# Kernel tuning notes

Measured on AMD Instinct MI355X. Metric: run time of the kernel, lower is better.

## Reference

```python
import jax, jax.numpy as jnp
import numpy as np

N, E, D, C, H1 = 50000, 800000, 128, 8, 2


def setup_inputs() -> dict:
    key = jax.random.key(0)
    ks = jax.random.split(key, 14)
    s = lambda k, sh: (jax.random.normal(k, sh, jnp.float32) * 0.05)
    return {
        "x": jax.random.normal(ks[0], (N, D), jnp.float32),
        "edge_index": jax.random.randint(ks[1], (2, E), 0, N, dtype=jnp.int32),
        # conv1: GATConv(D, D, heads=2, concat=True)
        "W1": s(ks[2], (D, H1 * D)),
        "att1_src": s(ks[3], (H1, D)),
        "att1_dst": s(ks[4], (H1, D)),
        "b1": s(ks[5], (H1 * D,)),
        # conv2: GATConv(2D, D, heads=1, concat=False)
        "W2": s(ks[6], (H1 * D, D)),
        "att2_src": s(ks[7], (1, D)),
        "att2_dst": s(ks[8], (1, D)),
        "b2": s(ks[9], (D,)),
        # MLP head
        "Wm1": s(ks[10], (D, D)),
        "bm1": s(ks[11], (D,)),
        "Wm2": s(ks[12], (D, C)),
        "bm2": s(ks[13], (C,)),
    }


def gat_conv(x, src, dst, W, a_src, a_dst, b, heads, out_ch, concat):
    """PyG GATConv (eval mode): self-loops added by caller, softmax over
    edges grouped by destination node, negative_slope=0.2."""
    n = x.shape[0]
    h = (x @ W).reshape(n, heads, out_ch)              # [N,H,F]
    alpha_src = jnp.einsum('nhf,hf->nh', h, a_src)     # [N,H]
    alpha_dst = jnp.einsum('nhf,hf->nh', h, a_dst)     # [N,H]
    e = jax.nn.leaky_relu(alpha_src[src] + alpha_dst[dst], 0.2)  # [E,H]
    e_max = jax.ops.segment_max(e, dst, num_segments=n)
    ex = jnp.exp(e - e_max[dst])
    denom = jax.ops.segment_sum(ex, dst, num_segments=n)
    alpha = ex / jnp.maximum(denom[dst], 1e-16)        # [E,H]
    out = jax.ops.segment_sum(h[src] * alpha[:, :, None], dst, num_segments=n)
    out = out.reshape(n, heads * out_ch) if concat else out.mean(axis=1)
    return out + b


def reference(x, edge_index, W1, att1_src, att1_dst, b1,
              W2, att2_src, att2_dst, b2, Wm1, bm1, Wm2, bm2):
    n = x.shape[0]
    loop = jnp.arange(n, dtype=edge_index.dtype)
    src = jnp.concatenate([edge_index[0], loop])  # add_self_loops=True
    dst = jnp.concatenate([edge_index[1], loop])
    h = jax.nn.elu(gat_conv(x, src, dst, W1, att1_src, att1_dst, b1, H1, D, True))
    h = jax.nn.elu(gat_conv(h, src, dst, W2, att2_src, att2_dst, b2, 1, D, False))
    h = jax.nn.relu(h @ Wm1 + bm1)
    return jax.nn.relu(h @ Wm2 + bm2)
```

## Files before the change

kernel.cpp:

```cpp
#include <hip/hip_runtime.h>
#include <hip/hip_bf16.h>


__device__ __forceinline__ float lrelu(float x){ return x > 0.f ? x : 0.2f*x; }
__device__ __forceinline__ float elu_f(float x){ return x > 0.f ? x : __expf(x) - 1.f; }
__device__ __forceinline__ unsigned short f2bf(float f){
  __hip_bfloat16 h = __float2bfloat16(f);
  return *reinterpret_cast<unsigned short*>(&h);
}
__device__ __forceinline__ float bflo(unsigned int u){ return __uint_as_float(u << 16); }
__device__ __forceinline__ float bfhi(unsigned int u){ return __uint_as_float(u & 0xffff0000u); }
__device__ __forceinline__ unsigned int packbf(float a, float b){
  return (unsigned int)f2bf(a) | ((unsigned int)f2bf(b) << 16);
}

typedef __attribute__((ext_vector_type(8))) short bf16x8;
typedef __attribute__((ext_vector_type(4))) float f32x4;

__global__ void prep_kernel(const float* __restrict__ W1, unsigned short* __restrict__ BT1a,
                            unsigned short* __restrict__ BT1b,
                            const float* __restrict__ W2, unsigned short* __restrict__ BT2,
                            const float* __restrict__ Wm1, unsigned short* __restrict__ BT3,
                            const float* __restrict__ a1s, const float* __restrict__ a1d,
                            float* __restrict__ va, int* __restrict__ bcount,
                            int* __restrict__ gcur, int NB){
  int idx = blockIdx.x*256 + threadIdx.x;
  const int S1 = 128*128, S2 = 128*256, S3 = 128*128;
  if (idx < S1){
    int n = idx >> 7, k = idx & 127;
    BT1a[idx] = f2bf(W1[(size_t)k*256 + n]);
    BT1b[idx] = f2bf(W1[(size_t)k*256 + 128 + n]);
  } else if (idx < S1 + S2){
    int j = idx - S1;
    int n = j >> 8, k = j & 255;
    BT2[j] = f2bf(W2[(size_t)k*128 + n]);
  } else if (idx < S1 + S2 + S3){
    int j = idx - S1 - S2;
    int n = j >> 7, k = j & 127;
    BT3[j] = f2bf(Wm1[(size_t)k*128 + n]);
  } else if (idx < S1 + S2 + S3 + 512){
    int j = idx - S1 - S2 - S3;
    int v = j >> 7, k = j & 127;
    const float* avec = (v < 2) ? a1s : a1d;
    int head = v & 1;
    const float* wrow = W1 + (size_t)k*256 + head*128;
    const float* arow = avec + head*128;
    float s = 0.f;
    #pragma unroll 8
    for (int f = 0; f < 128; ++f) s += wrow[f]*arow[f];
    va[j] = s;
  } else if (idx < S1 + S2 + S3 + 512 + 2048){
    int z = idx - (S1 + S2 + S3 + 512);
    if (z < 1024){ if (z < NB) bcount[z] = 0; }
    else { z -= 1024; if (z < NB) gcur[z] = 0; }
  }
}

__global__ __launch_bounds__(256) void f2bf_hist_kernel(
    const float* __restrict__ x, unsigned short* __restrict__ xb, int N,
    const float* __restrict__ va, float* __restrict__ as1, float* __restrict__ ad1,
    const int* __restrict__ dst, int E, int* __restrict__ bcount, int NB, int nbConv)
{
  __shared__ int h[1024];
  if ((int)blockIdx.x < nbConv){
    int i = blockIdx.x*256 + threadIdx.x;
    int total = N*32;
    float4 v = make_float4(0.f,0.f,0.f,0.f);
    if (i < total){
      v = ((const float4*)x)[i];
      ushort4 u; u.x=f2bf(v.x); u.y=f2bf(v.y); u.z=f2bf(v.z); u.w=f2bf(v.w);
      ((ushort4*)xb)[i] = u;
    }
    int c = (i & 31) << 2;
    float4 vs0 = *(const float4*)(va + c);
    float4 vs1 = *(const float4*)(va + 128 + c);
    float4 vd0 = *(const float4*)(va + 256 + c);
    float4 vd1 = *(const float4*)(va + 384 + c);
    float s0 = v.x*vs0.x + v.y*vs0.y + v.z*vs0.z + v.w*vs0.w;
    float s1 = v.x*vs1.x + v.y*vs1.y + v.z*vs1.z + v.w*vs1.w;
    float d0 = v.x*vd0.x + v.y*vd0.y + v.z*vd0.z + v.w*vd0.w;
    float d1 = v.x*vd1.x + v.y*vd1.y + v.z*vd1.z + v.w*vd1.w;
    #pragma unroll
    for (int m = 1; m <= 16; m <<= 1){
      s0 += __shfl_xor(s0, m); s1 += __shfl_xor(s1, m);
      d0 += __shfl_xor(d0, m); d1 += __shfl_xor(d1, m);
    }
    if ((i & 31) == 0 && i < total){
      int n = i >> 5;
      *(float2*)(as1 + 2*n) = make_float2(s0, s1);
      *(float2*)(ad1 + 2*n) = make_float2(d0, d1);
    }
  } else {
    for (int i = threadIdx.x; i < NB; i += 256) h[i] = 0;
    __syncthreads();
    int b0 = blockIdx.x - nbConv;
    for (int e = b0*256 + threadIdx.x; e < E; e += 64*256)
      atomicAdd(&h[dst[e] >> 6], 1);
    __syncthreads();
    for (int i = threadIdx.x; i < NB; i += 256)
      if (h[i]) atomicAdd(&bcount[i], h[i]);
  }
}

__global__ __launch_bounds__(256) void bscatter_kernel(
    const int* __restrict__ src, const int* __restrict__ dst, int E,
    const int* __restrict__ bcount, int* __restrict__ gcur,
    unsigned int* __restrict__ pairs, int* __restrict__ boff, int NB)
{
  __shared__ int h[1024];
  __shared__ int runbase[1024];
  __shared__ int sc[1024];
  const int t = threadIdx.x;

  #pragma unroll
  for (int q = 0; q < 4; ++q){
    int i = t + q*256;
    sc[i] = (i < NB) ? bcount[i] : 0;
  }
  __syncthreads();
  for (int d = 1; d < 1024; d <<= 1){
    int v[4];
    #pragma unroll
    for (int q = 0; q < 4; ++q){
      int idx = t + q*256;
      v[q] = (idx >= d) ? sc[idx - d] : 0;
    }
    __syncthreads();
    #pragma unroll
    for (int q = 0; q < 4; ++q) sc[t + q*256] += v[q];
    __syncthreads();
  }
  if (blockIdx.x == 0){
    for (int i = t; i < NB; i += 256) boff[i] = i ? sc[i-1] : 0;
    if (t == 0) boff[NB] = sc[NB-1];
  }

  const int e0 = blockIdx.x * 4096;
  for (int i = t; i < NB; i += 256) h[i] = 0;
  __syncthreads();
  int myb[16]; unsigned int myw[16];
  #pragma unroll
  for (int q = 0; q < 16; ++q){
    int e = e0 + q*256 + t;
    int b = -1; unsigned int w = 0;
    if (e < E){
      int d = dst[e];
      b = d >> 6;
      w = ((unsigned int)(d & 63) << 26) | (unsigned int)src[e];
      atomicAdd(&h[b], 1);
    }
    myb[q] = b; myw[q] = w;
  }
  __syncthreads();
  for (int i = t; i < NB; i += 256)
    runbase[i] = h[i] ? atomicAdd(&gcur[i], h[i]) : 0;
  __syncthreads();
  for (int i = t; i < NB; i += 256) h[i] = 0;
  __syncthreads();
  #pragma unroll
  for (int q = 0; q < 16; ++q){
    if (myb[q] >= 0){
      int off = atomicAdd(&h[myb[q]], 1);
      int base = myb[q] ? sc[myb[q]-1] : 0;
      pairs[(size_t)base + runbase[myb[q]] + off] = myw[q];
    }
  }
}

__global__ __launch_bounds__(256) void bbuild_kernel(
    const unsigned int* __restrict__ pairs, const int* __restrict__ boff,
    int* __restrict__ rowptr, int* __restrict__ csr, int N)
{
  __shared__ int deg[64], offs[64], cur[64];
  const int b = blockIdx.x;
  const int t = threadIdx.x;
  const int n0 = b << 6;
  const int nNodes = min(64, N - n0);
  const int p0 = boff[b], p1 = boff[b+1];
  const int base = p0 + n0;
  if (t < 64) deg[t] = (t < nNodes) ? 1 : 0;
  __syncthreads();
  for (int i = p0 + t; i < p1; i += 256)
    atomicAdd(&deg[pairs[i] >> 26], 1);
  __syncthreads();
  if (t < 64){
    int x = deg[t];
    #pragma unroll
    for (int d = 1; d < 64; d <<= 1){
      int y = __shfl_up(x, d);
      if (t >= d) x += y;
    }
    offs[t] = x - deg[t];
    cur[t] = 1;
    if (t < nNodes){
      rowptr[n0 + t + 1] = base + x;
      csr[base + x - deg[t]] = n0 + t;
    }
    if (b == 0 && t == 0) rowptr[0] = 0;
  }
  __syncthreads();
  for (int i = p0 + t; i < p1; i += 256){
    unsigned int w = pairs[i];
    int dl = w >> 26;
    int s  = (int)(w & 0x03ffffffu);
    int off = atomicAdd(&cur[dl], 1);
    csr[base + offs[dl] + off] = s;
  }
}

__device__ __forceinline__ void gemm_core(
    const unsigned short* __restrict__ A, int lda,
    const unsigned short* __restrict__ BT, int M, int K, int r0,
    unsigned short* a_s, unsigned short* b_s, f32x4 (&acc)[4][4])
{
  const int tid  = threadIdx.x;
  const int lane = tid & 63, wv = tid >> 6;
  const int mh = (wv & 1)*64, nh = (wv >> 1)*64;
  const int l15 = lane & 15, quad = lane >> 4;
  const int srow = tid >> 3, skc = tid & 7;

  #pragma unroll
  for (int i = 0; i < 4; ++i)
    #pragma unroll
    for (int j = 0; j < 4; ++j)
      #pragma unroll
      for (int r = 0; r < 4; ++r) acc[i][j][r] = 0.f;

  for (int k0 = 0; k0 < K; k0 += 64){
    #pragma unroll
    for (int it = 0; it < 4; ++it){
      int row = it*32 + srow;
      int grow = r0 + row;
      uint4 v = make_uint4(0u,0u,0u,0u);
      if (grow < M) v = *(const uint4*)(A + (size_t)grow*lda + k0 + skc*8);
      *(uint4*)(&a_s[row*72 + skc*8]) = v;
    }
    #pragma unroll
    for (int it = 0; it < 4; ++it){
      int row = it*32 + srow;
      uint4 v = *(const uint4*)(BT + (size_t)row*K + k0 + skc*8);
      *(uint4*)(&b_s[row*72 + skc*8]) = v;
    }
    __syncthreads();
    #pragma unroll
    for (int ks = 0; ks < 64; ks += 32){
      bf16x8 af[4], bfr[4];
      #pragma unroll
      for (int i = 0; i < 4; ++i)
        af[i] = *(const bf16x8*)(&a_s[(mh + i*16 + l15)*72 + ks + quad*8]);
      #pragma unroll
      for (int j = 0; j < 4; ++j)
        bfr[j] = *(const bf16x8*)(&b_s[(nh + j*16 + l15)*72 + ks + quad*8]);
      #pragma unroll
      for (int i = 0; i < 4; ++i)
        #pragma unroll
        for (int j = 0; j < 4; ++j)
          acc[i][j] = __builtin_amdgcn_mfma_f32_16x16x32_bf16(bfr[j], af[i], acc[i][j], 0, 0, 0);
    }
    __syncthreads();
  }
}

__global__ __launch_bounds__(256) void gemm_conv1_kernel(
    const unsigned short* __restrict__ xa, const unsigned short* __restrict__ BT1a,
    const unsigned short* __restrict__ BT1b, unsigned short* __restrict__ out1b,
    int M, const float* __restrict__ b1)
{
  __shared__ unsigned short a_s[128*72];
  __shared__ unsigned short b_s[128*72];
  const int hx = blockIdx.x;
  const unsigned short* A  = xa + hx*128;
  const unsigned short* BT = hx ? BT1b : BT1a;
  unsigned short* C = out1b + hx*128;
  const float* bias = b1 + hx*128;
  const int r0 = blockIdx.y*128;
  f32x4 acc[4][4];
  gemm_core(A, 256, BT, M, 128, r0, a_s, b_s, acc);

  const int lane = threadIdx.x & 63, wv = threadIdx.x >> 6;
  const int mh = (wv & 1)*64, nh = (wv >> 1)*64;
  const int l15 = lane & 15, quad = lane >> 4;
  #pragma unroll
  for (int i = 0; i < 4; ++i){
    int m = r0 + mh + i*16 + l15;
    if (m < M){
      #pragma unroll
      for (int j = 0; j < 4; ++j){
        int n = nh + j*16 + quad*4;
        float4 bb = *(const float4*)(bias + n);
        ushort4 u;
        u.x = f2bf(elu_f(acc[i][j][0] + bb.x));
        u.y = f2bf(elu_f(acc[i][j][1] + bb.y));
        u.z = f2bf(elu_f(acc[i][j][2] + bb.z));
        u.w = f2bf(elu_f(acc[i][j][3] + bb.w));
        *(ushort4*)(C + (size_t)m*256 + n) = u;
      }
    }
  }
}

__global__ __launch_bounds__(256) void gemm_conv2_kernel(
    const unsigned short* __restrict__ out1b, const unsigned short* __restrict__ BT2,
    unsigned short* __restrict__ h2b, int M,
    const float* __restrict__ a2s, const float* __restrict__ a2d,
    float* __restrict__ as2, float* __restrict__ ad2)
{
  __shared__ unsigned short a_s[128*72];
  __shared__ unsigned short b_s[128*72];
  __shared__ float part_s[128][2];
  __shared__ float part_d[128][2];
  const int r0 = blockIdx.y*128;
  f32x4 acc[4][4];
  gemm_core(out1b, 256, BT2, M, 256, r0, a_s, b_s, acc);

  const int tid = threadIdx.x;
  const int lane = tid & 63, wv = tid >> 6;
  const int mh = (wv & 1)*64, nh = (wv >> 1)*64;
  const int l15 = lane & 15, quad = lane >> 4;
  #pragma unroll
  for (int i = 0; i < 4; ++i){
    int m = r0 + mh + i*16 + l15;
    float ps = 0.f, pd = 0.f;
    #pragma unroll
    for (int j = 0; j < 4; ++j){
      int n = nh + j*16 + quad*4;
      float4 wsv = *(const float4*)(a2s + n);
      float4 wdv = *(const float4*)(a2d + n);
      float v0 = acc[i][j][0], v1 = acc[i][j][1], v2 = acc[i][j][2], v3 = acc[i][j][3];
      ps += v0*wsv.x + v1*wsv.y + v2*wsv.z + v3*wsv.w;
      pd += v0*wdv.x + v1*wdv.y + v2*wdv.z + v3*wdv.w;
      if (m < M){
        ushort4 u;
        u.x = f2bf(v0); u.y = f2bf(v1); u.z = f2bf(v2); u.w = f2bf(v3);
        *(ushort4*)(h2b + (size_t)m*128 + n) = u;
      }
    }
    ps += __shfl_xor(ps, 16); ps += __shfl_xor(ps, 32);
    pd += __shfl_xor(pd, 16); pd += __shfl_xor(pd, 32);
    if (quad == 0){
      part_s[mh + i*16 + l15][wv >> 1] = ps;
      part_d[mh + i*16 + l15][wv >> 1] = pd;
    }
  }
  __syncthreads();
  if (tid < 128){
    int gm = r0 + tid;
    if (gm < M){
      as2[gm] = part_s[tid][0] + part_s[tid][1];
      ad2[gm] = part_d[tid][0] + part_d[tid][1];
    }
  }
}

__global__ __launch_bounds__(256) void gemm_mlp_kernel(
    const unsigned short* __restrict__ gb, const unsigned short* __restrict__ BT3,
    int M, const float* __restrict__ bm1, const float* __restrict__ Wm2,
    const float* __restrict__ bm2, float* __restrict__ out)
{
  __shared__ unsigned short a_s[128*72];
  __shared__ unsigned short b_s[128*72];
  __shared__ float wm2_s[128*8];
  __shared__ float part[128][2][8];
  const int tid = threadIdx.x;
  {
    int i4 = tid*4;
    *(float4*)(&wm2_s[i4]) = *(const float4*)(Wm2 + i4);
  }
  const int r0 = blockIdx.y*128;
  f32x4 acc[4][4];
  gemm_core(gb, 128, BT3, M, 128, r0, a_s, b_s, acc);

  const int lane = tid & 63, wv = tid >> 6;
  const int mh = (wv & 1)*64, nh = (wv >> 1)*64;
  const int l15 = lane & 15, quad = lane >> 4;
  #pragma unroll
  for (int i = 0; i < 4; ++i){
    float po[8];
    #pragma unroll
    for (int o = 0; o < 8; ++o) po[o] = 0.f;
    #pragma unroll
    for (int j = 0; j < 4; ++j){
      int n = nh + j*16 + quad*4;
      float4 bb = *(const float4*)(bm1 + n);
      #pragma unroll
      for (int r = 0; r < 4; ++r){
        float hcol = fmaxf(acc[i][j][r] + ((const float*)&bb)[r], 0.f);
        const float* wr = &wm2_s[(n + r)*8];
        #pragma unroll
        for (int o = 0; o < 8; ++o) po[o] += hcol*wr[o];
      }
    }
    #pragma unroll
    for (int o = 0; o < 8; ++o){
      po[o] += __shfl_xor(po[o], 16);
      po[o] += __shfl_xor(po[o], 32);
    }
    if (quad == 0){
      #pragma unroll
      for (int o = 0; o < 8; ++o) part[mh + i*16 + l15][wv >> 1][o] = po[o];
    }
  }
  __syncthreads();
  if (tid < 128){
    int gm = r0 + tid;
    if (gm < M){
      float4 o0, o1;
      o0.x = fmaxf(part[tid][0][0] + part[tid][1][0] + bm2[0], 0.f);
      o0.y = fmaxf(part[tid][0][1] + part[tid][1][1] + bm2[1], 0.f);
      o0.z = fmaxf(part[tid][0][2] + part[tid][1][2] + bm2[2], 0.f);
      o0.w = fmaxf(part[tid][0][3] + part[tid][1][3] + bm2[3], 0.f);
      o1.x = fmaxf(part[tid][0][4] + part[tid][1][4] + bm2[4], 0.f);
      o1.y = fmaxf(part[tid][0][5] + part[tid][1][5] + bm2[5], 0.f);
      o1.z = fmaxf(part[tid][0][6] + part[tid][1][6] + bm2[6], 0.f);
      o1.w = fmaxf(part[tid][0][7] + part[tid][1][7] + bm2[7], 0.f);
      *(float4*)(out + (size_t)gm*8)     = o0;
      *(float4*)(out + (size_t)gm*8 + 4) = o1;
    }
  }
}

__global__ __launch_bounds__(256) void agg1x_kernel(
    const unsigned short* __restrict__ xb, const float* __restrict__ as_,
    const float* __restrict__ ad_, const int* __restrict__ rowptr, const int* __restrict__ csr,
    unsigned short* __restrict__ xa, int N)
{
  const int wv = threadIdx.x >> 6, lane = threadIdx.x & 63;
  const int ql = lane & 15;
  const int n = blockIdx.x*16 + wv*4 + (lane >> 4);
  const bool valid = n < N;
  int start = 0, end = 0;
  float2 adv = make_float2(0.f, 0.f);
  if (valid){ start = rowptr[n]; end = rowptr[n+1]; adv = *(const float2*)(ad_ + 2*n); }

  int jl = start + ql;
  bool have = valid && (jl < end);
  int s_l = 0;
  float p0 = 0.f, p1 = 0.f;
  if (have){
    s_l = csr[jl];
    float2 av = *(const float2*)(as_ + 2*s_l);
    p0 = __expf(lrelu(av.x + adv.x));
    p1 = __expf(lrelu(av.y + adv.y));
  }
  float l0 = p0, l1 = p1;
  for (int j = jl + 16; j < end; j += 16){
    int s = csr[j];
    float2 av = *(const float2*)(as_ + 2*s);
    l0 += __expf(lrelu(av.x + adv.x));
    l1 += __expf(lrelu(av.y + adv.y));
  }
  #pragma unroll
  for (int msk = 1; msk <= 8; msk <<= 1){
    l0 += __shfl_xor(l0, msk);
    l1 += __shfl_xor(l1, msk);
  }
  float inv0 = 1.f / fmaxf(l0, 1e-16f);
  float inv1 = 1.f / fmaxf(l1, 1e-16f);
  float a0_l = p0 * inv0;
  float a1_l = p1 * inv1;

  float acc0[8], acc1[8];
  #pragma unroll
  for (int i = 0; i < 8; ++i){ acc0[i] = 0.f; acc1[i] = 0.f; }
  const int c = ql << 3;
  const unsigned short* hp = xb + c;

  int cnt = valid ? min(16, end - start) : 0;
  int t = 0;
  for (; t + 3 < cnt; t += 4){
    int   sA  = __shfl(s_l, t, 16),    sB  = __shfl(s_l, t+1, 16);
    int   sC  = __shfl(s_l, t+2, 16),  sD  = __shfl(s_l, t+3, 16);
    float a0A = __shfl(a0_l, t, 16),   a0B = __shfl(a0_l, t+1, 16);
    float a0C = __shfl(a0_l, t+2, 16), a0D = __shfl(a0_l, t+3, 16);
    float a1A = __shfl(a1_l, t, 16),   a1B = __shfl(a1_l, t+1, 16);
    float a1C = __shfl(a1_l, t+2, 16), a1D = __shfl(a1_l, t+3, 16);
    uint4 uA = *(const uint4*)(hp + (sA << 7));
    uint4 uB = *(const uint4*)(hp + (sB << 7));
    uint4 uC = *(const uint4*)(hp + (sC << 7));
    uint4 uD = *(const uint4*)(hp + (sD << 7));
    float fA[8] = {bflo(uA.x),bfhi(uA.x),bflo(uA.y),bfhi(uA.y),bflo(uA.z),bfhi(uA.z),bflo(uA.w),bfhi(uA.w)};
    float fB[8] = {bflo(uB.x),bfhi(uB.x),bflo(uB.y),bfhi(uB.y),bflo(uB.z),bfhi(uB.z),bflo(uB.w),bfhi(uB.w)};
    float fC[8] = {bflo(uC.x),bfhi(uC.x),bflo(uC.y),bfhi(uC.y),bflo(uC.z),bfhi(uC.z),bflo(uC.w),bfhi(uC.w)};
    float fD[8] = {bflo(uD.x),bfhi(uD.x),bflo(uD.y),bfhi(uD.y),bflo(uD.z),bfhi(uD.z),bflo(uD.w),bfhi(uD.w)};
    #pragma unroll
    for (int i = 0; i < 8; ++i){
      acc0[i] += a0A*fA[i] + a0B*fB[i] + a0C*fC[i] + a0D*fD[i];
      acc1[i] += a1A*fA[i] + a1B*fB[i] + a1C*fC[i] + a1D*fD[i];
    }
  }
  for (; t < cnt; ++t){
    int   sA  = __shfl(s_l, t, 16);
    float a0A = __shfl(a0_l, t, 16);
    float a1A = __shfl(a1_l, t, 16);
    uint4 u = *(const uint4*)(hp + (sA << 7));
    float fA[8] = {bflo(u.x),bfhi(u.x),bflo(u.y),bfhi(u.y),bflo(u.z),bfhi(u.z),bflo(u.w),bfhi(u.w)};
    #pragma unroll
    for (int i = 0; i < 8; ++i){
      acc0[i] += a0A*fA[i];
      acc1[i] += a1A*fA[i];
    }
  }
  for (int jb = start + 16; jb < end; jb += 16){
    int jl2 = jb + ql;
    int s2 = 0; float a0_2 = 0.f, a1_2 = 0.f;
    if (jl2 < end){
      s2 = csr[jl2];
      float2 av = *(const float2*)(as_ + 2*s2);
      a0_2 = __expf(lrelu(av.x + adv.x)) * inv0;
      a1_2 = __expf(lrelu(av.y + adv.y)) * inv1;
    }
    int cnt2 = min(16, end - jb);
    for (int t2 = 0; t2 < cnt2; ++t2){
      int   sA  = __shfl(s2, t2, 16);
      float a0A = __shfl(a0_2, t2, 16);
      float a1A = __shfl(a1_2, t2, 16);
      uint4 u = *(const uint4*)(hp + (sA << 7));
      float fA[8] = {bflo(u.x),bfhi(u.x),bflo(u.y),bfhi(u.y),bflo(u.z),bfhi(u.z),bflo(u.w),bfhi(u.w)};
      #pragma unroll
      for (int i = 0; i < 8; ++i){
        acc0[i] += a0A*fA[i];
        acc1[i] += a1A*fA[i];
      }
    }
  }

  if (valid){
    uint4 u0, u1;
    u0.x = packbf(acc0[0], acc0[1]); u0.y = packbf(acc0[2], acc0[3]);
    u0.z = packbf(acc0[4], acc0[5]); u0.w = packbf(acc0[6], acc0[7]);
    u1.x = packbf(acc1[0], acc1[1]); u1.y = packbf(acc1[2], acc1[3]);
    u1.z = packbf(acc1[4], acc1[5]); u1.w = packbf(acc1[6], acc1[7]);
    *(uint4*)(xa + (size_t)n*256 + c)       = u0;
    *(uint4*)(xa + (size_t)n*256 + 128 + c) = u1;
  }
}

__global__ __launch_bounds__(256) void agg2_kernel(
    const unsigned short* __restrict__ h2b, const float* __restrict__ as_,
    const float* __restrict__ ad_, const int* __restrict__ rowptr, const int* __restrict__ csr,
    const float* __restrict__ b2, unsigned short* __restrict__ outb, int N)
{
  const int wv = threadIdx.x >> 6, lane = threadIdx.x & 63;
  const int ql = lane & 15;
  const int n = blockIdx.x*16 + wv*4 + (lane >> 4);
  const bool valid = n < N;
  int start = 0, end = 0;
  float adn = 0.f;
  if (valid){ start = rowptr[n]; end = rowptr[n+1]; adn = ad_[n]; }

  int jl = start + ql;
  bool have = valid && (jl < end);
  int s_l = 0;
  float p_l = 0.f;
  if (have){
    s_l = csr[jl];
    p_l = __expf(lrelu(as_[s_l] + adn));
  }
  float l = p_l;
  for (int j = jl + 16; j < end; j += 16)
    l += __expf(lrelu(as_[csr[j]] + adn));
  #pragma unroll
  for (int msk = 1; msk <= 8; msk <<= 1) l += __shfl_xor(l, msk);
  float inv = 1.f / fmaxf(l, 1e-16f);
  float a_l = p_l * inv;

  float acc[8];
  #pragma unroll
  for (int i = 0; i < 8; ++i) acc[i] = 0.f;
  const int c = ql << 3;
  const unsigned short* hp = h2b + c;

  int cnt = valid ? min(16, end - start) : 0;
  int t = 0;
  for (; t + 3 < cnt; t += 4){
    int   sA = __shfl(s_l, t, 16),   sB = __shfl(s_l, t+1, 16);
    int   sC = __shfl(s_l, t+2, 16), sD = __shfl(s_l, t+3, 16);
    float aA = __shfl(a_l, t, 16),   aB = __shfl(a_l, t+1, 16);
    float aC = __shfl(a_l, t+2, 16), aD = __shfl(a_l, t+3, 16);
    uint4 uA = *(const uint4*)(hp + (sA << 7));
    uint4 uB = *(const uint4*)(hp + (sB << 7));
    uint4 uC = *(const uint4*)(hp + (sC << 7));
    uint4 uD = *(const uint4*)(hp + (sD << 7));
    float fA[8] = {bflo(uA.x),bfhi(uA.x),bflo(uA.y),bfhi(uA.y),bflo(uA.z),bfhi(uA.z),bflo(uA.w),bfhi(uA.w)};
    float fB[8] = {bflo(uB.x),bfhi(uB.x),bflo(uB.y),bfhi(uB.y),bflo(uB.z),bfhi(uB.z),bflo(uB.w),bfhi(uB.w)};
    float fC[8] = {bflo(uC.x),bfhi(uC.x),bflo(uC.y),bfhi(uC.y),bflo(uC.z),bfhi(uC.z),bflo(uC.w),bfhi(uC.w)};
    float fD[8] = {bflo(uD.x),bfhi(uD.x),bflo(uD.y),bfhi(uD.y),bflo(uD.z),bfhi(uD.z),bflo(uD.w),bfhi(uD.w)};
    #pragma unroll
    for (int i = 0; i < 8; ++i)
      acc[i] += aA*fA[i] + aB*fB[i] + aC*fC[i] + aD*fD[i];
  }
  for (; t < cnt; ++t){
    int   sA = __shfl(s_l, t, 16);
    float aA = __shfl(a_l, t, 16);
    uint4 u = *(const uint4*)(hp + (sA << 7));
    float fA[8] = {bflo(u.x),bfhi(u.x),bflo(u.y),bfhi(u.y),bflo(u.z),bfhi(u.z),bflo(u.w),bfhi(u.w)};
    #pragma unroll
    for (int i = 0; i < 8; ++i) acc[i] += aA*fA[i];
  }
  for (int jb = start + 16; jb < end; jb += 16){
    int jl2 = jb + ql;
    int s2 = 0; float a2 = 0.f;
    if (jl2 < end){
      s2 = csr[jl2];
      a2 = __expf(lrelu(as_[s2] + adn)) * inv;
    }
    int cnt2 = min(16, end - jb);
    for (int t2 = 0; t2 < cnt2; ++t2){
      int   sA = __shfl(s2, t2, 16);
      float aA = __shfl(a2, t2, 16);
      uint4 u = *(const uint4*)(hp + (sA << 7));
      float fA[8] = {bflo(u.x),bfhi(u.x),bflo(u.y),bfhi(u.y),bflo(u.z),bfhi(u.z),bflo(u.w),bfhi(u.w)};
      #pragma unroll
      for (int i = 0; i < 8; ++i) acc[i] += aA*fA[i];
    }
  }

  if (valid){
    float4 bb0 = *(const float4*)(b2 + c);
    float4 bb1 = *(const float4*)(b2 + c + 4);
    float o[8];
    o[0]=elu_f(acc[0]+bb0.x); o[1]=elu_f(acc[1]+bb0.y);
    o[2]=elu_f(acc[2]+bb0.z); o[3]=elu_f(acc[3]+bb0.w);
    o[4]=elu_f(acc[4]+bb1.x); o[5]=elu_f(acc[5]+bb1.y);
    o[6]=elu_f(acc[6]+bb1.z); o[7]=elu_f(acc[7]+bb1.w);
    uint4 up;
    up.x = packbf(o[0], o[1]); up.y = packbf(o[2], o[3]);
    up.z = packbf(o[4], o[5]); up.w = packbf(o[6], o[7]);
    *(uint4*)(outb + (size_t)n*128 + c) = up;
  }
}

extern "C" void kernel_launch(void* const* d_in, const int* in_sizes, int n_in,
                              void* d_out, int out_size, void* d_ws, size_t ws_size,
                              hipStream_t stream)
{
  (void)n_in; (void)out_size; (void)ws_size;
  const float* x   = (const float*)d_in[0];
  const int*   ei  = (const int*)d_in[1];
  const float* W1  = (const float*)d_in[2];
  const float* a1s = (const float*)d_in[3];
  const float* a1d = (const float*)d_in[4];
  const float* b1  = (const float*)d_in[5];
  const float* W2  = (const float*)d_in[6];
  const float* a2s = (const float*)d_in[7];
  const float* a2d = (const float*)d_in[8];
  const float* b2  = (const float*)d_in[9];
  const float* Wm1 = (const float*)d_in[10];
  const float* bm1 = (const float*)d_in[11];
  const float* Wm2 = (const float*)d_in[12];
  const float* bm2 = (const float*)d_in[13];
  float* out = (float*)d_out;

  const int N = in_sizes[0] / 128;
  const int E = in_sizes[1] / 2;
  const int NB = (N + 63) >> 6;
  const int* srcp = ei;
  const int* dstp = ei + E;

  char* ws = (char*)d_ws;
  unsigned short* xb    = (unsigned short*)ws;
  unsigned short* xa    = (unsigned short*)(ws + (size_t)N*256);
  unsigned short* out1b = (unsigned short*)(ws + (size_t)N*768);
  unsigned short* h2b   = (unsigned short*)(ws + (size_t)N*1280);
  char* tail = ws + (size_t)N*1536;
  unsigned short* BT1a = (unsigned short*)tail;
  unsigned short* BT1b = BT1a + 128*128;
  unsigned short* BT2  = BT1b + 128*128;
  unsigned short* BT3  = BT2 + 128*256;
  float* va   = (float*)(BT3 + 128*128);
  float* as1  = va + 512;
  float* ad1  = as1 + (size_t)2*N;
  float* as2  = ad1 + (size_t)2*N;
  float* ad2  = as2 + N;
  int* bcount = (int*)(ad2 + N);
  int* boff   = bcount + 1024;
  int* gcur   = boff + 1032;
  int* rowptr = gcur + 1024;
  int* csr    = rowptr + N + 1;
  unsigned int* pairs = (unsigned int*)(csr + E + N);

  unsigned short* gb = xb;

  const int nbConv = (N*32 + 255)/256;
  const int prepTotal = 128*128 + 128*256 + 128*128 + 512 + 2048;

  prep_kernel<<<(prepTotal + 255)/256, 256, 0, stream>>>(
      W1, BT1a, BT1b, W2, BT2, Wm1, BT3, a1s, a1d, va, bcount, gcur, NB);
  f2bf_hist_kernel<<<nbConv + 64, 256, 0, stream>>>(x, xb, N, va, as1, ad1,
                                                    dstp, E, bcount, NB, nbConv);
  bscatter_kernel<<<(E + 4095)/4096, 256, 0, stream>>>(srcp, dstp, E, bcount, gcur,
                                                       pairs, boff, NB);
  bbuild_kernel<<<NB, 256, 0, stream>>>(pairs, boff, rowptr, csr, N);

  const int gy   = (N + 127) / 128;
  const int nb16 = (N + 15) / 16;

  agg1x_kernel<<<nb16, 256, 0, stream>>>(xb, as1, ad1, rowptr, csr, xa, N);
  gemm_conv1_kernel<<<dim3(2, gy), 256, 0, stream>>>(xa, BT1a, BT1b, out1b, N, b1);
  gemm_conv2_kernel<<<dim3(1, gy), 256, 0, stream>>>(out1b, BT2, h2b, N, a2s, a2d, as2, ad2);
  agg2_kernel<<<nb16, 256, 0, stream>>>(h2b, as2, ad2, rowptr, csr, b2, gb, N);
  gemm_mlp_kernel<<<dim3(1, gy), 256, 0, stream>>>(gb, BT3, N, bm1, Wm2, bm2, out);
}
```

Before: 267.7 us.

## Fuse layer-2 aggregation with the MLP head GEMM into one kernel

Merges the conv2 neighbor aggregation and the MLP head into a single kernel. Each block of 256 threads aggregates 128 destination rows in 8 passes, writing bf16 results straight into shared memory, then runs the MFMA GEMM with Wm1 and the Wm2 projection from there. This drops one launch and the global write and read of the intermediate N×128 bf16 buffer. In exchange, each block now has only 128 rows of gather work with a barrier before the GEMM, so there are fewer, larger blocks and gather latency may be hidden less well.

```diff
diff --git a/kernel.cpp b/kernel.cpp
--- a/kernel.cpp
+++ b/kernel.cpp
@@ -352,27 +352,157 @@
   }
 }
 
-__global__ __launch_bounds__(256) void gemm_mlp_kernel(
-    const unsigned short* __restrict__ gb, const unsigned short* __restrict__ BT3,
-    int M, const float* __restrict__ bm1, const float* __restrict__ Wm2,
-    const float* __restrict__ bm2, float* __restrict__ out)
-{
-  __shared__ unsigned short a_s[128*72];
+__global__ __launch_bounds__(256) void agg2_mlp_kernel(
+    const unsigned short* __restrict__ h2b, const float* __restrict__ as_,
+    const float* __restrict__ ad_, const int* __restrict__ rowptr,
+    const int* __restrict__ csr, const float* __restrict__ b2,
+    const unsigned short* __restrict__ BT3, int N, const float* __restrict__ bm1,
+    const float* __restrict__ Wm2, const float* __restrict__ bm2,
+    float* __restrict__ out)
+{
+  __shared__ unsigned short a_s[128*136];
   __shared__ unsigned short b_s[128*72];
-  __shared__ float wm2_s[128*8];
-  __shared__ float part[128][2][8];
   const int tid = threadIdx.x;
+  const int wv = tid >> 6, lane = tid & 63;
+  const int ql = lane & 15;
+  const int grp = wv*4 + (lane >> 4);
+  const int r0 = blockIdx.x*128;
+
+  for (int pass = 0; pass < 8; ++pass){
+    const int row = pass*16 + grp;
+    const int n = r0 + row;
+    const bool valid = n < N;
+    int start = 0, end = 0;
+    float adn = 0.f;
+    if (valid){ start = rowptr[n]; end = rowptr[n+1]; adn = ad_[n]; }
+
+    int jl = start + ql;
+    bool have = valid && (jl < end);
+    int s_l = 0;
+    float p_l = 0.f;
+    if (have){
+      s_l = csr[jl];
+      p_l = __expf(lrelu(as_[s_l] + adn));
+    }
+    float l = p_l;
+    for (int j = jl + 16; j < end; j += 16)
+      l += __expf(lrelu(as_[csr[j]] + adn));
+    #pragma unroll
+    for (int msk = 1; msk <= 8; msk <<= 1) l += __shfl_xor(l, msk);
+    float inv = 1.f / fmaxf(l, 1e-16f);
+    float a_l = p_l * inv;
+
+    float acc[8];
+    #pragma unroll
+    for (int i = 0; i < 8; ++i) acc[i] = 0.f;
+    const int c = ql << 3;
+    const unsigned short* hp = h2b + c;
+
+    int cnt = valid ? min(16, end - start) : 0;
+    int t = 0;
+    for (; t + 3 < cnt; t += 4){
+      int   sA = __shfl(s_l, t, 16),   sB = __shfl(s_l, t+1, 16);
+      int   sC = __shfl(s_l, t+2, 16), sD = __shfl(s_l, t+3, 16);
+      float aA = __shfl(a_l, t, 16),   aB = __shfl(a_l, t+1, 16);
+      float aC = __shfl(a_l, t+2, 16), aD = __shfl(a_l, t+3, 16);
+      uint4 uA = *(const uint4*)(hp + (sA << 7));
+      uint4 uB = *(const uint4*)(hp + (sB << 7));
+      uint4 uC = *(const uint4*)(hp + (sC << 7));
+      uint4 uD = *(const uint4*)(hp + (sD << 7));
+      float fA[8] = {bflo(uA.x),bfhi(uA.x),bflo(uA.y),bfhi(uA.y),bflo(uA.z),bfhi(uA.z),bflo(uA.w),bfhi(uA.w)};
+      float fB[8] = {bflo(uB.x),bfhi(uB.x),bflo(uB.y),bfhi(uB.y),bflo(uB.z),bfhi(uB.z),bflo(uB.w),bfhi(uB.w)};
+      float fC[8] = {bflo(uC.x),bfhi(uC.x),bflo(uC.y),bfhi(uC.y),bflo(uC.z),bfhi(uC.z),bflo(uC.w),bfhi(uC.w)};
+      float fD[8] = {bflo(uD.x),bfhi(uD.x),bflo(uD.y),bfhi(uD.y),bflo(uD.z),bfhi(uD.z),bflo(uD.w),bfhi(uD.w)};
+      #pragma unroll
+      for (int i = 0; i < 8; ++i)
+        acc[i] += aA*fA[i] + aB*fB[i] + aC*fC[i] + aD*fD[i];
+    }
+    for (; t < cnt; ++t){
+      int   sA = __shfl(s_l, t, 16);
+      float aA = __shfl(a_l, t, 16);
+      uint4 u = *(const uint4*)(hp + (sA << 7));
+      float fA[8] = {bflo(u.x),bfhi(u.x),bflo(u.y),bfhi(u.y),bflo(u.z),bfhi(u.z),bflo(u.w),bfhi(u.w)};
+      #pragma unroll
+      for (int i = 0; i < 8; ++i) acc[i] += aA*fA[i];
+    }
+    for (int jb = start + 16; jb < end; jb += 16){
+      int jl2 = jb + ql;
+      int s2 = 0; float a2 = 0.f;
+      if (jl2 < end){
+        s2 = csr[jl2];
+        a2 = __expf(lrelu(as_[s2] + adn)) * inv;
+      }
+      int cnt2 = min(16, end - jb);
+      for (int t2 = 0; t2 < cnt2; ++t2){
+        int   sA = __shfl(s2, t2, 16);
+        float aA = __shfl(a2, t2, 16);
+        uint4 u = *(const uint4*)(hp + (sA << 7));
+        float fA[8] = {bflo(u.x),bfhi(u.x),bflo(u.y),bfhi(u.y),bflo(u.z),bfhi(u.z),bflo(u.w),bfhi(u.w)};
+        #pragma unroll
+        for (int i = 0; i < 8; ++i) acc[i] += aA*fA[i];
+      }
+    }
+
+    uint4 up = make_uint4(0u,0u,0u,0u);
+    if (valid){
+      float4 bb0 = *(const float4*)(b2 + c);
+      float4 bb1 = *(const float4*)(b2 + c + 4);
+      float o[8];
+      o[0]=elu_f(acc[0]+bb0.x); o[1]=elu_f(acc[1]+bb0.y);
+      o[2]=elu_f(acc[2]+bb0.z); o[3]=elu_f(acc[3]+bb0.w);
+      o[4]=elu_f(acc[4]+bb1.x); o[5]=elu_f(acc[5]+bb1.y);
+      o[6]=elu_f(acc[6]+bb1.z); o[7]=elu_f(acc[7]+bb1.w);
+      up.x = packbf(o[0], o[1]); up.y = packbf(o[2], o[3]);
+      up.z = packbf(o[4], o[5]); up.w = packbf(o[6], o[7]);
+    }
+    *(uint4*)(&a_s[row*136 + c]) = up;
+  }
+  __syncthreads();
+
+  const int mh = (wv & 1)*64, nh = (wv >> 1)*64;
+  const int l15 = lane & 15, quad = lane >> 4;
+  const int srow = tid >> 3, skc = tid & 7;
+  f32x4 acc[4][4];
+  #pragma unroll
+  for (int i = 0; i < 4; ++i)
+    #pragma unroll
+    for (int j = 0; j < 4; ++j)
+      #pragma unroll
+      for (int r = 0; r < 4; ++r) acc[i][j][r] = 0.f;
+
+  for (int k0 = 0; k0 < 128; k0 += 64){
+    #pragma unroll
+    for (int it = 0; it < 4; ++it){
+      int rowb = it*32 + srow;
+      uint4 v = *(const uint4*)(BT3 + (size_t)rowb*128 + k0 + skc*8);
+      *(uint4*)(&b_s[rowb*72 + skc*8]) = v;
+    }
+    __syncthreads();
+    #pragma unroll
+    for (int ks = 0; ks < 64; ks += 32){
+      bf16x8 af[4], bfr[4];
+      #pragma unroll
+      for (int i = 0; i < 4; ++i)
+        af[i] = *(const bf16x8*)(&a_s[(mh + i*16 + l15)*136 + k0 + ks + quad*8]);
+      #pragma unroll
+      for (int j = 0; j < 4; ++j)
+        bfr[j] = *(const bf16x8*)(&b_s[(nh + j*16 + l15)*72 + ks + quad*8]);
+      #pragma unroll
+      for (int i = 0; i < 4; ++i)
+        #pragma unroll
+        for (int j = 0; j < 4; ++j)
+          acc[i][j] = __builtin_amdgcn_mfma_f32_16x16x32_bf16(bfr[j], af[i], acc[i][j], 0, 0, 0);
+    }
+    __syncthreads();
+  }
+
+  float* wm2_s = (float*)b_s;
+  float* part  = ((float*)b_s) + 1024;
   {
     int i4 = tid*4;
     *(float4*)(&wm2_s[i4]) = *(const float4*)(Wm2 + i4);
   }
-  const int r0 = blockIdx.y*128;
-  f32x4 acc[4][4];
-  gemm_core(gb, 128, BT3, M, 128, r0, a_s, b_s, acc);
-
-  const int lane = tid & 63, wv = tid >> 6;
-  const int mh = (wv & 1)*64, nh = (wv >> 1)*64;
-  const int l15 = lane & 15, quad = lane >> 4;
+  __syncthreads();
   #pragma unroll
   for (int i = 0; i < 4; ++i){
     float po[8];
@@ -397,22 +527,23 @@
     }
     if (quad == 0){
       #pragma unroll
-      for (int o = 0; o < 8; ++o) part[mh + i*16 + l15][wv >> 1][o] = po[o];
+      for (int o = 0; o < 8; ++o)
+        part[(mh + i*16 + l15)*16 + (wv >> 1)*8 + o] = po[o];
     }
   }
   __syncthreads();
   if (tid < 128){
     int gm = r0 + tid;
-    if (gm < M){
+    if (gm < N){
       float4 o0, o1;
-      o0.x = fmaxf(part[tid][0][0] + part[tid][1][0] + bm2[0], 0.f);
-      o0.y = fmaxf(part[tid][0][1] + part[tid][1][1] + bm2[1], 0.f);
-      o0.z = fmaxf(part[tid][0][2] + part[tid][1][2] + bm2[2], 0.f);
-      o0.w = fmaxf(part[tid][0][3] + part[tid][1][3] + bm2[3], 0.f);
-      o1.x = fmaxf(part[tid][0][4] + part[tid][1][4] + bm2[4], 0.f);
-      o1.y = fmaxf(part[tid][0][5] + part[tid][1][5] + bm2[5], 0.f);
-      o1.z = fmaxf(part[tid][0][6] + part[tid][1][6] + bm2[6], 0.f);
-      o1.w = fmaxf(part[tid][0][7] + part[tid][1][7] + bm2[7], 0.f);
+      o0.x = fmaxf(part[tid*16 + 0] + part[tid*16 + 8]  + bm2[0], 0.f);
+      o0.y = fmaxf(part[tid*16 + 1] + part[tid*16 + 9]  + bm2[1], 0.f);
+      o0.z = fmaxf(part[tid*16 + 2] + part[tid*16 + 10] + bm2[2], 0.f);
+      o0.w = fmaxf(part[tid*16 + 3] + part[tid*16 + 11] + bm2[3], 0.f);
+      o1.x = fmaxf(part[tid*16 + 4] + part[tid*16 + 12] + bm2[4], 0.f);
+      o1.y = fmaxf(part[tid*16 + 5] + part[tid*16 + 13] + bm2[5], 0.f);
+      o1.z = fmaxf(part[tid*16 + 6] + part[tid*16 + 14] + bm2[6], 0.f);
+      o1.w = fmaxf(part[tid*16 + 7] + part[tid*16 + 15] + bm2[7], 0.f);
       *(float4*)(out + (size_t)gm*8)     = o0;
       *(float4*)(out + (size_t)gm*8 + 4) = o1;
     }
@@ -532,101 +663,6 @@
     u1.z = packbf(acc1[4], acc1[5]); u1.w = packbf(acc1[6], acc1[7]);
     *(uint4*)(xa + (size_t)n*256 + c)       = u0;
     *(uint4*)(xa + (size_t)n*256 + 128 + c) = u1;
-  }
-}
-
-__global__ __launch_bounds__(256) void agg2_kernel(
-    const unsigned short* __restrict__ h2b, const float* __restrict__ as_,
-    const float* __restrict__ ad_, const int* __restrict__ rowptr, const int* __restrict__ csr,
-    const float* __restrict__ b2, unsigned short* __restrict__ outb, int N)
-{
-  const int wv = threadIdx.x >> 6, lane = threadIdx.x & 63;
-  const int ql = lane & 15;
-  const int n = blockIdx.x*16 + wv*4 + (lane >> 4);
-  const bool valid = n < N;
-  int start = 0, end = 0;
-  float adn = 0.f;
-  if (valid){ start = rowptr[n]; end = rowptr[n+1]; adn = ad_[n]; }
-
-  int jl = start + ql;
-  bool have = valid && (jl < end);
-  int s_l = 0;
-  float p_l = 0.f;
-  if (have){
-    s_l = csr[jl];
-    p_l = __expf(lrelu(as_[s_l] + adn));
-  }
-  float l = p_l;
-  for (int j = jl + 16; j < end; j += 16)
-    l += __expf(lrelu(as_[csr[j]] + adn));
-  #pragma unroll
-  for (int msk = 1; msk <= 8; msk <<= 1) l += __shfl_xor(l, msk);
-  float inv = 1.f / fmaxf(l, 1e-16f);
-  float a_l = p_l * inv;
-
-  float acc[8];
-  #pragma unroll
-  for (int i = 0; i < 8; ++i) acc[i] = 0.f;
-  const int c = ql << 3;
-  const unsigned short* hp = h2b + c;
-
-  int cnt = valid ? min(16, end - start) : 0;
-  int t = 0;
-  for (; t + 3 < cnt; t += 4){
-    int   sA = __shfl(s_l, t, 16),   sB = __shfl(s_l, t+1, 16);
-    int   sC = __shfl(s_l, t+2, 16), sD = __shfl(s_l, t+3, 16);
-    float aA = __shfl(a_l, t, 16),   aB = __shfl(a_l, t+1, 16);
-    float aC = __shfl(a_l, t+2, 16), aD = __shfl(a_l, t+3, 16);
-    uint4 uA = *(const uint4*)(hp + (sA << 7));
-    uint4 uB = *(const uint4*)(hp + (sB << 7));
-    uint4 uC = *(const uint4*)(hp + (sC << 7));
-    uint4 uD = *(const uint4*)(hp + (sD << 7));
-    float fA[8] = {bflo(uA.x),bfhi(uA.x),bflo(uA.y),bfhi(uA.y),bflo(uA.z),bfhi(uA.z),bflo(uA.w),bfhi(uA.w)};
-    float fB[8] = {bflo(uB.x),bfhi(uB.x),bflo(uB.y),bfhi(uB.y),bflo(uB.z),bfhi(uB.z),bflo(uB.w),bfhi(uB.w)};
-    float fC[8] = {bflo(uC.x),bfhi(uC.x),bflo(uC.y),bfhi(uC.y),bflo(uC.z),bfhi(uC.z),bflo(uC.w),bfhi(uC.w)};
-    float fD[8] = {bflo(uD.x),bfhi(uD.x),bflo(uD.y),bfhi(uD.y),bflo(uD.z),bfhi(uD.z),bflo(uD.w),bfhi(uD.w)};
-    #pragma unroll
-    for (int i = 0; i < 8; ++i)
-      acc[i] += aA*fA[i] + aB*fB[i] + aC*fC[i] + aD*fD[i];
-  }
-  for (; t < cnt; ++t){
-    int   sA = __shfl(s_l, t, 16);
-    float aA = __shfl(a_l, t, 16);
-    uint4 u = *(const uint4*)(hp + (sA << 7));
-    float fA[8] = {bflo(u.x),bfhi(u.x),bflo(u.y),bfhi(u.y),bflo(u.z),bfhi(u.z),bflo(u.w),bfhi(u.w)};
-    #pragma unroll
-    for (int i = 0; i < 8; ++i) acc[i] += aA*fA[i];
-  }
-  for (int jb = start + 16; jb < end; jb += 16){
-    int jl2 = jb + ql;
-    int s2 = 0; float a2 = 0.f;
-    if (jl2 < end){
-      s2 = csr[jl2];
-      a2 = __expf(lrelu(as_[s2] + adn)) * inv;
-    }
-    int cnt2 = min(16, end - jb);
-    for (int t2 = 0; t2 < cnt2; ++t2){
-      int   sA = __shfl(s2, t2, 16);
-      float aA = __shfl(a2, t2, 16);
-      uint4 u = *(const uint4*)(hp + (sA << 7));
-      float fA[8] = {bflo(u.x),bfhi(u.x),bflo(u.y),bfhi(u.y),bflo(u.z),bfhi(u.z),bflo(u.w),bfhi(u.w)};
-      #pragma unroll
-      for (int i = 0; i < 8; ++i) acc[i] += aA*fA[i];
-    }
-  }
-
-  if (valid){
-    float4 bb0 = *(const float4*)(b2 + c);
-    float4 bb1 = *(const float4*)(b2 + c + 4);
-    float o[8];
-    o[0]=elu_f(acc[0]+bb0.x); o[1]=elu_f(acc[1]+bb0.y);
-    o[2]=elu_f(acc[2]+bb0.z); o[3]=elu_f(acc[3]+bb0.w);
-    o[4]=elu_f(acc[4]+bb1.x); o[5]=elu_f(acc[5]+bb1.y);
-    o[6]=elu_f(acc[6]+bb1.z); o[7]=elu_f(acc[7]+bb1.w);
-    uint4 up;
-    up.x = packbf(o[0], o[1]); up.y = packbf(o[2], o[3]);
-    up.z = packbf(o[4], o[5]); up.w = packbf(o[6], o[7]);
-    *(uint4*)(outb + (size_t)n*128 + c) = up;
   }
 }
 
@@ -679,8 +715,6 @@
   int* csr    = rowptr + N + 1;
   unsigned int* pairs = (unsigned int*)(csr + E + N);
 
-  unsigned short* gb = xb;
-
   const int nbConv = (N*32 + 255)/256;
   const int prepTotal = 128*128 + 128*256 + 128*128 + 512 + 2048;
 
@@ -698,6 +732,6 @@
   agg1x_kernel<<<nb16, 256, 0, stream>>>(xb, as1, ad1, rowptr, csr, xa, N);
   gemm_conv1_kernel<<<dim3(2, gy), 256, 0, stream>>>(xa, BT1a, BT1b, out1b, N, b1);
   gemm_conv2_kernel<<<dim3(1, gy), 256, 0, stream>>>(out1b, BT2, h2b, N, a2s, a2d, as2, ad2);
-  agg2_kernel<<<nb16, 256, 0, stream>>>(h2b, as2, ad2, rowptr, csr, b2, gb, N);
-  gemm_mlp_kernel<<<dim3(1, gy), 256, 0, stream>>>(gb, BT3, N, bm1, Wm2, bm2, out);
-}
+  agg2_mlp_kernel<<<gy, 256, 0, stream>>>(h2b, as2, ad2, rowptr, csr, b2,
+                                          BT3, N, bm1, Wm2, bm2, out);
+}
```

Result: slower. 295.3 us (+10.3%).

## Fuse layer-2 aggregation with MLP head into a single kernel

Applied to the files above, without the earlier changes.

Merges the second GAT aggregation kernel with the MLP head. Each block of 16 nodes stages its ELU outputs in shared memory, runs the 128x128 Wm1 GEMM with 16x16x32 bf16 MFMAs, and then computes the 8-wide output layer in shared memory. This removes one launch and the global write and re-read of the N x 128 bf16 intermediate. In exchange, the MLP GEMM now works on small 16-row tiles that read BT3 straight from global/L2 for every block, and the extra shared memory may lower occupancy of the latency-bound gather loop.

```diff
diff --git a/kernel.cpp b/kernel.cpp
--- a/kernel.cpp
+++ b/kernel.cpp
@@ -352,73 +352,6 @@
   }
 }
 
-__global__ __launch_bounds__(256) void gemm_mlp_kernel(
-    const unsigned short* __restrict__ gb, const unsigned short* __restrict__ BT3,
-    int M, const float* __restrict__ bm1, const float* __restrict__ Wm2,
-    const float* __restrict__ bm2, float* __restrict__ out)
-{
-  __shared__ unsigned short a_s[128*72];
-  __shared__ unsigned short b_s[128*72];
-  __shared__ float wm2_s[128*8];
-  __shared__ float part[128][2][8];
-  const int tid = threadIdx.x;
-  {
-    int i4 = tid*4;
-    *(float4*)(&wm2_s[i4]) = *(const float4*)(Wm2 + i4);
-  }
-  const int r0 = blockIdx.y*128;
-  f32x4 acc[4][4];
-  gemm_core(gb, 128, BT3, M, 128, r0, a_s, b_s, acc);
-
-  const int lane = tid & 63, wv = tid >> 6;
-  const int mh = (wv & 1)*64, nh = (wv >> 1)*64;
-  const int l15 = lane & 15, quad = lane >> 4;
-  #pragma unroll
-  for (int i = 0; i < 4; ++i){
-    float po[8];
-    #pragma unroll
-    for (int o = 0; o < 8; ++o) po[o] = 0.f;
-    #pragma unroll
-    for (int j = 0; j < 4; ++j){
-      int n = nh + j*16 + quad*4;
-      float4 bb = *(const float4*)(bm1 + n);
-      #pragma unroll
-      for (int r = 0; r < 4; ++r){
-        float hcol = fmaxf(acc[i][j][r] + ((const float*)&bb)[r], 0.f);
-        const float* wr = &wm2_s[(n + r)*8];
-        #pragma unroll
-        for (int o = 0; o < 8; ++o) po[o] += hcol*wr[o];
-      }
-    }
-    #pragma unroll
-    for (int o = 0; o < 8; ++o){
-      po[o] += __shfl_xor(po[o], 16);
-      po[o] += __shfl_xor(po[o], 32);
-    }
-    if (quad == 0){
-      #pragma unroll
-      for (int o = 0; o < 8; ++o) part[mh + i*16 + l15][wv >> 1][o] = po[o];
-    }
-  }
-  __syncthreads();
-  if (tid < 128){
-    int gm = r0 + tid;
-    if (gm < M){
-      float4 o0, o1;
-      o0.x = fmaxf(part[tid][0][0] + part[tid][1][0] + bm2[0], 0.f);
-      o0.y = fmaxf(part[tid][0][1] + part[tid][1][1] + bm2[1], 0.f);
-      o0.z = fmaxf(part[tid][0][2] + part[tid][1][2] + bm2[2], 0.f);
-      o0.w = fmaxf(part[tid][0][3] + part[tid][1][3] + bm2[3], 0.f);
-      o1.x = fmaxf(part[tid][0][4] + part[tid][1][4] + bm2[4], 0.f);
-      o1.y = fmaxf(part[tid][0][5] + part[tid][1][5] + bm2[5], 0.f);
-      o1.z = fmaxf(part[tid][0][6] + part[tid][1][6] + bm2[6], 0.f);
-      o1.w = fmaxf(part[tid][0][7] + part[tid][1][7] + bm2[7], 0.f);
-      *(float4*)(out + (size_t)gm*8)     = o0;
-      *(float4*)(out + (size_t)gm*8 + 4) = o1;
-    }
-  }
-}
-
 __global__ __launch_bounds__(256) void agg1x_kernel(
     const unsigned short* __restrict__ xb, const float* __restrict__ as_,
     const float* __restrict__ ad_, const int* __restrict__ rowptr, const int* __restrict__ csr,
@@ -535,15 +468,29 @@
   }
 }
 
-__global__ __launch_bounds__(256) void agg2_kernel(
+__global__ __launch_bounds__(256) void agg2_mlp_kernel(
     const unsigned short* __restrict__ h2b, const float* __restrict__ as_,
-    const float* __restrict__ ad_, const int* __restrict__ rowptr, const int* __restrict__ csr,
-    const float* __restrict__ b2, unsigned short* __restrict__ outb, int N)
-{
-  const int wv = threadIdx.x >> 6, lane = threadIdx.x & 63;
+    const float* __restrict__ ad_, const int* __restrict__ rowptr,
+    const int* __restrict__ csr, const float* __restrict__ b2,
+    const unsigned short* __restrict__ BT3, int N, const float* __restrict__ bm1,
+    const float* __restrict__ Wm2, const float* __restrict__ bm2,
+    float* __restrict__ out)
+{
+  __shared__ unsigned short g_s[16*136];
+  __shared__ float h_s[16*132];
+  __shared__ float wm2_s[128*8];
+  const int tid = threadIdx.x;
+  const int wv = tid >> 6, lane = tid & 63;
   const int ql = lane & 15;
-  const int n = blockIdx.x*16 + wv*4 + (lane >> 4);
+  const int grp = wv*4 + (lane >> 4);
+  const int n = blockIdx.x*16 + grp;
   const bool valid = n < N;
+
+  {
+    int i4 = tid*4;
+    *(float4*)(&wm2_s[i4]) = *(const float4*)(Wm2 + i4);
+  }
+
   int start = 0, end = 0;
   float adn = 0.f;
   if (valid){ start = rowptr[n]; end = rowptr[n+1]; adn = ad_[n]; }
@@ -615,6 +562,7 @@
     }
   }
 
+  uint4 up = make_uint4(0u,0u,0u,0u);
   if (valid){
     float4 bb0 = *(const float4*)(b2 + c);
     float4 bb1 = *(const float4*)(b2 + c + 4);
@@ -623,10 +571,51 @@
     o[2]=elu_f(acc[2]+bb0.z); o[3]=elu_f(acc[3]+bb0.w);
     o[4]=elu_f(acc[4]+bb1.x); o[5]=elu_f(acc[5]+bb1.y);
     o[6]=elu_f(acc[6]+bb1.z); o[7]=elu_f(acc[7]+bb1.w);
-    uint4 up;
     up.x = packbf(o[0], o[1]); up.y = packbf(o[2], o[3]);
     up.z = packbf(o[4], o[5]); up.w = packbf(o[6], o[7]);
-    *(uint4*)(outb + (size_t)n*128 + c) = up;
+  }
+  *(uint4*)(&g_s[grp*136 + c]) = up;
+  __syncthreads();
+
+  const int l15 = lane & 15, quad = lane >> 4;
+  f32x4 macc[2];
+  #pragma unroll
+  for (int j = 0; j < 2; ++j)
+    #pragma unroll
+    for (int r = 0; r < 4; ++r) macc[j][r] = 0.f;
+  #pragma unroll
+  for (int ks = 0; ks < 128; ks += 32){
+    bf16x8 af = *(const bf16x8*)(&g_s[l15*136 + ks + quad*8]);
+    #pragma unroll
+    for (int j = 0; j < 2; ++j){
+      int n2 = wv*32 + j*16 + l15;
+      bf16x8 bf = *(const bf16x8*)(BT3 + (size_t)n2*128 + ks + quad*8);
+      macc[j] = __builtin_amdgcn_mfma_f32_16x16x32_bf16(bf, af, macc[j], 0, 0, 0);
+    }
+  }
+  #pragma unroll
+  for (int j = 0; j < 2; ++j){
+    #pragma unroll
+    for (int r = 0; r < 4; ++r){
+      int n2 = wv*32 + j*16 + quad*4 + r;
+      h_s[l15*132 + n2] = fmaxf(macc[j][r] + bm1[n2], 0.f);
+    }
+  }
+  __syncthreads();
+
+  {
+    const int node = tid >> 4;
+    const int rem  = tid & 15;
+    const int o    = rem >> 1;
+    const int kg   = rem & 1;
+    const float* hrow = &h_s[node*132 + kg*64];
+    float po = 0.f;
+    #pragma unroll 16
+    for (int k = 0; k < 64; ++k) po += hrow[k] * wm2_s[(kg*64 + k)*8 + o];
+    po += __shfl_xor(po, 1);
+    int gm = blockIdx.x*16 + node;
+    if (kg == 0 && gm < N)
+      out[(size_t)gm*8 + o] = fmaxf(po + bm2[o], 0.f);
   }
 }
 
@@ -679,8 +668,6 @@
   int* csr    = rowptr + N + 1;
   unsigned int* pairs = (unsigned int*)(csr + E + N);
 
-  unsigned short* gb = xb;
-
   const int nbConv = (N*32 + 255)/256;
   const int prepTotal = 128*128 + 128*256 + 128*128 + 512 + 2048;
 
@@ -698,6 +685,6 @@
   agg1x_kernel<<<nb16, 256, 0, stream>>>(xb, as1, ad1, rowptr, csr, xa, N);
   gemm_conv1_kernel<<<dim3(2, gy), 256, 0, stream>>>(xa, BT1a, BT1b, out1b, N, b1);
   gemm_conv2_kernel<<<dim3(1, gy), 256, 0, stream>>>(out1b, BT2, h2b, N, a2s, a2d, as2, ad2);
-  agg2_kernel<<<nb16, 256, 0, stream>>>(h2b, as2, ad2, rowptr, csr, b2, gb, N);
-  gemm_mlp_kernel<<<dim3(1, gy), 256, 0, stream>>>(gb, BT3, N, bm1, Wm2, bm2, out);
-}
+  agg2_mlp_kernel<<<nb16, 256, 0, stream>>>(h2b, as2, ad2, rowptr, csr, b2,
+                                            BT3, N, bm1, Wm2, bm2, out);
+}
```

Measured after the change: 274.8 us. 2.7% more time.
